# Optimization experiments

Hardware: AMD Instinct MI355X
Metric: run time of the kernel (lower is better)

The kernel has to match this reference:

```python
import jax, jax.numpy as jnp
import numpy as np

N_HEADS = 16

def setup_inputs() -> dict:
    key = jax.random.key(0)
    k1, k2, k3, k4 = jax.random.split(key, 4)
    B, T, C = 2, 2048, 1024
    x = jax.random.normal(k1, (B, T, C), dtype=jnp.float32)
    # torch nn.Linear weights: (out_features, in_features), applied as x @ W.T
    s = 1.0 / np.sqrt(C)
    Wq = jax.random.normal(k2, (C, C), dtype=jnp.float32) * s
    Wk = jax.random.normal(k3, (C, C), dtype=jnp.float32) * s
    Wv = jax.random.normal(k4, (C, C), dtype=jnp.float32) * s
    return {"x": x, "Wq": Wq, "Wk": Wk, "Wv": Wv}

def reference(x, Wq, Wk, Wv):
    B, T, C = x.shape
    H = N_HEADS
    d = C // H
    q = (x @ Wq.T).reshape(B, T, H, d)
    k = (x @ Wk.T).reshape(B, T, H, d)
    v = (x @ Wv.T).reshape(B, T, H, d)
    # NOTE: original scales by full C**-0.5, not per-head dim
    wei = jnp.einsum('bqhd,bkhd->bhqk', q, k) * (C ** -0.5)
    causal = jnp.tril(jnp.ones((T, T), dtype=bool))
    wei = jnp.where(causal, wei, -jnp.inf)
    wei = jax.nn.softmax(wei, axis=-1)
    out = jnp.einsum('bhqk,bkhd->bqhd', wei, v)
    return out.reshape(B, T, C)
```

## Files before the change

kernel.cpp:

```cpp
#include <hip/hip_runtime.h>
#include <math.h>

typedef __attribute__((ext_vector_type(8))) short short8;
typedef __attribute__((ext_vector_type(4))) float f32x4;
typedef __attribute__((ext_vector_type(16))) float f32x16;

#define BDIM 2
#define T_LEN 2048
#define CDIM 1024
#define NH 16
#define DHEAD 64
#define M_ROWS (BDIM * T_LEN)
#define NX (M_ROWS * CDIM)
#define NW (CDIM * CDIM)

#define QSCL 0.045084220f

__device__ inline unsigned short f2bf(float f) {
    union { float f; unsigned u; } v; v.f = f;
    unsigned r = v.u + 0x7fff + ((v.u >> 16) & 1);
    return (unsigned short)(r >> 16);
}

__device__ __forceinline__ void gload16(const unsigned short* g, unsigned short* l) {
    __builtin_amdgcn_global_load_lds(
        (const __attribute__((address_space(1))) void*)g,
        (__attribute__((address_space(3))) void*)l, 16, 0, 0);
}

__global__ __launch_bounds__(256) void conv_bf16(
    const float* __restrict__ x, const float* __restrict__ wq,
    const float* __restrict__ wk, const float* __restrict__ wv,
    unsigned short* __restrict__ dst)
{
    int id = blockIdx.x * 256 + threadIdx.x;
    const float* s;
    float scl = 1.0f;
    if (id < NX / 8) s = x + (size_t)id * 8;
    else {
        int r = id - NX / 8;
        int wsel = r >> 17;
        int off = r & 131071;
        const float* w = (wsel == 0) ? wq : (wsel == 1) ? wk : wv;
        if (wsel == 0) scl = QSCL;
        s = w + (size_t)off * 8;
    }
    float4 a = ((const float4*)s)[0];
    float4 b = ((const float4*)s)[1];
    union { unsigned short u[8]; short8 v; } o;
    o.u[0] = f2bf(a.x * scl); o.u[1] = f2bf(a.y * scl); o.u[2] = f2bf(a.z * scl); o.u[3] = f2bf(a.w * scl);
    o.u[4] = f2bf(b.x * scl); o.u[5] = f2bf(b.y * scl); o.u[6] = f2bf(b.z * scl); o.u[7] = f2bf(b.w * scl);
    *(short8*)(dst + (size_t)id * 8) = o.v;
}

__global__ __launch_bounds__(256) void qkv_gemm_f(
    const unsigned short* __restrict__ xb, const unsigned short* __restrict__ wb,
    unsigned short* __restrict__ qkv)
{
    __shared__ unsigned short sh[17408];
    unsigned short* A = sh;
    unsigned short* Bt = sh + 8192;
    const int z = blockIdx.z;
    const int m0 = blockIdx.x * 128;
    const int n0 = blockIdx.y * 128;
    const int tid = threadIdx.x;
    const int l = tid & 63, w = tid >> 6;
    const int li = l & 15, g4 = l >> 4;
    const int wr = w >> 1, wc = w & 1;

    const unsigned short* wsrc = wb + (size_t)z * NW;
    f32x4 acc[4][4] = {};

    for (int k0 = 0; k0 < CDIM; k0 += 64) {
        __syncthreads();
        #pragma unroll
        for (int s = 0; s < 4; ++s) {
            int c = w * 256 + s * 64 + l;
            int row = c >> 3, wcol = c & 7;
            int sw = wcol ^ (row & 7);
            gload16(xb + (size_t)(m0 + row) * CDIM + k0 + sw * 8, A + (w * 256 + s * 64) * 8);
            gload16(wsrc + (size_t)(n0 + row) * CDIM + k0 + sw * 8, Bt + (w * 256 + s * 64) * 8);
        }
        asm volatile("s_waitcnt vmcnt(0)" ::: "memory");
        __syncthreads();
        __builtin_amdgcn_s_setprio(1);
        #pragma unroll
        for (int ks = 0; ks < 2; ++ks) {
            short8 af[4], bf[4];
            #pragma unroll
            for (int fm = 0; fm < 4; ++fm) {
                int row = wr * 64 + fm * 16 + li;
                int lin = row * 128 + ks * 64 + g4 * 16;
                af[fm] = *(const short8*)((const char*)A + (lin ^ ((row & 7) << 4)));
            }
            #pragma unroll
            for (int fn = 0; fn < 4; ++fn) {
                int row = wc * 64 + fn * 16 + li;
                int lin = row * 128 + ks * 64 + g4 * 16;
                bf[fn] = *(const short8*)((const char*)Bt + (lin ^ ((row & 7) << 4)));
            }
            #pragma unroll
            for (int fm = 0; fm < 4; ++fm)
                #pragma unroll
                for (int fn = 0; fn < 4; ++fn)
                    acc[fm][fn] = __builtin_amdgcn_mfma_f32_16x16x32_bf16(af[fm], bf[fn], acc[fm][fn], 0, 0, 0);
        }
        __builtin_amdgcn_s_setprio(0);
    }
    __syncthreads();

    if (z != 2) {
        unsigned short* outp = qkv + (size_t)z * NX;
        #pragma unroll
        for (int fm = 0; fm < 4; ++fm)
            #pragma unroll
            for (int fn = 0; fn < 4; ++fn)
                #pragma unroll
                for (int r = 0; r < 4; ++r) {
                    int m = m0 + wr * 64 + fm * 16 + g4 * 4 + r;
                    int n = n0 + wc * 64 + fn * 16 + li;
                    int b = m >> 11, t = m & 2047;
                    int h = n >> 6, dd = n & 63;
                    outp[((size_t)(b * NH + h) << 17) + ((size_t)t << 6) + dd] = f2bf(acc[fm][fn][r]);
                }
    } else {
        unsigned short (*T)[136] = (unsigned short(*)[136])sh;
        #pragma unroll
        for (int fm = 0; fm < 4; ++fm)
            #pragma unroll
            for (int fn = 0; fn < 4; ++fn)
                #pragma unroll
                for (int r = 0; r < 4; ++r) {
                    int ml = wr * 64 + fm * 16 + g4 * 4 + r;
                    int nl = wc * 64 + fn * 16 + li;
                    T[nl][ml] = f2bf(acc[fm][fn][r]);
                }
        __syncthreads();
        int b = m0 >> 11;
        int t0 = m0 & 2047;
        unsigned short* vt = qkv + 2 * (size_t)NX;
        #pragma unroll
        for (int s = 0; s < 8; ++s) {
            int row = tid >> 1;
            int col = ((tid & 1) * 8 + s) * 8;
            int ng = n0 + row;
            int h = ng >> 6, dd = ng & 63;
            *(short8*)(vt + ((size_t)(b * NH + h) * 64 + dd) * T_LEN + t0 + col)
                = *(const short8*)&T[row][col];
        }
    }
}

__global__ __launch_bounds__(512, 2) void attn(
    const unsigned short* __restrict__ qkv, float* __restrict__ out)
{
    __shared__ __align__(16) unsigned short KV[2][2][2][8192];

    const int id = blockIdx.x;
    const int half = id >> 8;
    const int rr = id & 255;
    const int tI = rr >> 5;
    const int bx = half ? tI : (15 - tI);
    const int rb = rr & 31;
    const int bh = (rb & 7) * 4 + (rb >> 3);
    const int b = bh >> 4, h = bh & 15;
    const int q0 = bx * 128;
    const int tid = threadIdx.x;
    const int l = tid & 63, w = tid >> 6;
    const int hf = w >> 2, chunk = w & 3;
    const int q31 = l & 31, hi = l >> 5;

    const unsigned short* qp = qkv + (size_t)bh * (T_LEN * DHEAD);
    const unsigned short* kp = qkv + (size_t)NX + (size_t)bh * (T_LEN * DHEAD);
    const unsigned short* vp = qkv + 2 * (size_t)NX + (size_t)bh * (T_LEN * DHEAD);

    const int q0w = q0 + chunk * 32;
    const int qg = q0w + q31;

    short8 aq[4];
    #pragma unroll
    for (int ks = 0; ks < 4; ++ks)
        aq[ks] = *(const short8*)(qp + (size_t)qg * DHEAD + ks * 16 + hi * 8);

    float m_run = -INFINITY, l_run = 0.f;
    f32x16 acc_o[2] = {};

    const int T128 = bx + 1;
    const int hA = (T128 + 1) >> 1;
    const int base = hf ? hA : 0;
    const int lim  = hf ? T128 : hA;
    const int nIt  = hA;
    const int myNt64 = 2 * bx + (chunk >> 1) + 1;

    auto STAGE = [&](int j, int bf) {
        const int kv0 = j * 128;
        #pragma unroll
        for (int s = 0; s < 4; ++s) {
            int g = (chunk * 4 + s) * 64 + l;
            int krow = g >> 3, kc = g & 7;
            int ksw = kc ^ (krow & 7);
            gload16(kp + (size_t)(kv0 + krow) * DHEAD + ksw * 8, &KV[hf][bf][0][(chunk * 4 + s) * 512]);
            int sub = g >> 9, cs = g & 511;
            int vrow = cs >> 3, vc = cs & 7;
            int vsw = vc ^ (vrow & 7);
            gload16(vp + (size_t)vrow * T_LEN + kv0 + sub * 64 + vsw * 8, &KV[hf][bf][1][(chunk * 4 + s) * 512]);
        }
    };

    if (base < lim) STAGE(base, 0);
    asm volatile("s_waitcnt vmcnt(0)" ::: "memory");
    __syncthreads();

    for (int i = 0; i < nIt; ++i) {
        const int cur = i & 1;
        const int myJ = base + i;
        if (myJ + 1 < lim) STAGE(myJ + 1, cur ^ 1);

        #pragma unroll
        for (int sub = 0; sub < 2; ++sub) {
            const int t64 = myJ * 2 + sub;
            if (myJ < lim && t64 < myNt64) {
                const char* Kbase = (const char*)&KV[hf][cur][0][0] + sub * 8192;
                const char* Vbase = (const char*)&KV[hf][cur][1][0] + sub * 8192;
                const int kv0 = t64 * 64;

                f32x16 sacc[2] = {};
                __builtin_amdgcn_s_setprio(1);
                #pragma unroll
                for (int ks = 0; ks < 4; ++ks) {
                    #pragma unroll
                    for (int nb = 0; nb < 2; ++nb) {
                        int row = 32 * nb + q31;
                        int lin = row * 128 + ks * 32 + hi * 16;
                        short8 ak = *(const short8*)(Kbase + (lin ^ ((l & 7) << 4)));
                        sacc[nb] = __builtin_amdgcn_mfma_f32_32x32x16_bf16(ak, aq[ks], sacc[nb], 0, 0, 0);
                    }
                }
                __builtin_amdgcn_s_setprio(0);

                const bool domask = (kv0 + 63 > q0w);
                if (domask) {
                    #pragma unroll
                    for (int nb = 0; nb < 2; ++nb)
                        #pragma unroll
                        for (int r = 0; r < 16; ++r) {
                            int kvg = kv0 + 32 * nb + (r & 3) + 8 * (r >> 2) + 4 * hi;
                            if (kvg > qg) sacc[nb][r] = -INFINITY;
                        }
                }
                float m16[16];
                #pragma unroll
                for (int r = 0; r < 16; ++r) m16[r] = fmaxf(sacc[0][r], sacc[1][r]);
                #pragma unroll
                for (int st = 8; st >= 1; st >>= 1)
                    #pragma unroll
                    for (int r2 = 0; r2 < 8; ++r2)
                        if (r2 < st) m16[r2] = fmaxf(m16[r2], m16[r2 + st]);
                float mloc = fmaxf(m16[0], __shfl_xor(m16[0], 32));

                bool upd = mloc > m_run + 8.0f;
                if (__any(upd)) {
                    float mn = fmaxf(m_run, mloc);
                    float c = exp2f(m_run - mn);
                    l_run *= c;
                    #pragma unroll
                    for (int nb2 = 0; nb2 < 2; ++nb2)
                        #pragma unroll
                        for (int r = 0; r < 16; ++r)
                            acc_o[nb2][r] *= c;
                    m_run = mn;
                }
                float ps[16];
                #pragma unroll
                for (int r = 0; r < 16; ++r) {
                    float p0 = exp2f(sacc[0][r] - m_run);
                    float p1 = exp2f(sacc[1][r] - m_run);
                    sacc[0][r] = p0; sacc[1][r] = p1;
                    ps[r] = p0 + p1;
                }
                #pragma unroll
                for (int st = 8; st >= 1; st >>= 1)
                    #pragma unroll
                    for (int r2 = 0; r2 < 8; ++r2)
                        if (r2 < st) ps[r2] += ps[r2 + st];
                l_run += ps[0] + __shfl_xor(ps[0], 32);

                unsigned dw[16];
                #pragma unroll
                for (int u = 0; u < 16; ++u) {
                    float lo = sacc[u >> 3][(2 * u) & 15];
                    float hif = sacc[u >> 3][((2 * u) & 15) + 1];
                    asm("v_cvt_pk_bf16_f32 %0, %1, %2" : "=v"(dw[u]) : "v"(lo), "v"(hif));
                }

                __builtin_amdgcn_s_setprio(1);
                #pragma unroll
                for (int ks = 0; ks < 4; ++ks) {
                    unsigned a0 = dw[4 * ks],     b0 = dw[4 * ks + 2];
                    unsigned a1 = dw[4 * ks + 1], b1 = dw[4 * ks + 3];
                    asm("v_permlane32_swap_b32 %0, %1" : "+v"(a0), "+v"(b0));
                    asm("v_permlane32_swap_b32 %0, %1" : "+v"(a1), "+v"(b1));
                    union { unsigned u[4]; short8 v; } pb;
                    pb.u[0] = a0; pb.u[1] = a1; pb.u[2] = b0; pb.u[3] = b1;
                    #pragma unroll
                    for (int nb2 = 0; nb2 < 2; ++nb2) {
                        int row = 32 * nb2 + q31;
                        int lin = row * 128 + ks * 32 + hi * 16;
                        short8 av = *(const short8*)(Vbase + (lin ^ ((l & 7) << 4)));
                        acc_o[nb2] = __builtin_amdgcn_mfma_f32_32x32x16_bf16(av, pb.v, acc_o[nb2], 0, 0, 0);
                    }
                }
                __builtin_amdgcn_s_setprio(0);
            }
        }
        asm volatile("s_waitcnt vmcnt(0)" ::: "memory");
        __syncthreads();
    }

    float* MB = (float*)&KV[0][0][0][0];
    float* slot = MB + (chunk * 64 + l) * 34;
    if (hf) {
        #pragma unroll
        for (int nb2 = 0; nb2 < 2; ++nb2)
            #pragma unroll
            for (int r = 0; r < 16; ++r) slot[nb2 * 16 + r] = acc_o[nb2][r];
        slot[32] = m_run; slot[33] = l_run;
    }
    __syncthreads();
    if (!hf) {
        float mB = slot[32], lB = slot[33];
        float m = fmaxf(m_run, mB);
        float cA = exp2f(m_run - m);
        float cB = (mB == -INFINITY) ? 0.f : exp2f(mB - m);
        float inv = 1.0f / (l_run * cA + lB * cB);
        float* ob = out + ((size_t)(b * T_LEN + qg)) * CDIM + h * DHEAD;
        #pragma unroll
        for (int nb2 = 0; nb2 < 2; ++nb2)
            #pragma unroll
            for (int r = 0; r < 16; ++r) {
                int dd = 32 * nb2 + (r & 3) + 8 * (r >> 2) + 4 * hi;
                ob[dd] = (acc_o[nb2][r] * cA + slot[nb2 * 16 + r] * cB) * inv;
            }
    }
}

extern "C" void kernel_launch(void* const* d_in, const int* in_sizes, int n_in,
                              void* d_out, int out_size, void* d_ws, size_t ws_size,
                              hipStream_t stream) {
    const float* x  = (const float*)d_in[0];
    const float* Wq = (const float*)d_in[1];
    const float* Wk = (const float*)d_in[2];
    const float* Wv = (const float*)d_in[3];
    float* out = (float*)d_out;

    unsigned short* xb = (unsigned short*)d_out;
    unsigned short* wb = xb + NX;
    unsigned short* qkv = (unsigned short*)d_ws;

    conv_bf16<<<dim3((NX / 8 + 3 * NW / 8) / 256), dim3(256), 0, stream>>>(x, Wq, Wk, Wv, xb);
    qkv_gemm_f<<<dim3(M_ROWS / 128, CDIM / 128, 3), dim3(256), 0, stream>>>(xb, wb, qkv);
    attn<<<dim3(512), dim3(512), 0, stream>>>(qkv, out);
}
```

Measured before the change: 102.1 us.

## Process full 128-wide KV tile per softmax step with split PV accumulators

Each iteration now computes QK^T scores for the whole 128-key staged tile at once, instead of two sequential 64-key halves. That halves the per-tile max/sum reductions, cross-lane shuffles and rescale checks. The P·V products for the two halves go into separate accumulators, summed at the end, so the two halves' MFMA chains do not depend on each other. In exchange, register pressure rises (four score accumulators plus two output accumulators), and on the diagonal some fully masked 64-key halves are now computed instead of skipped.

```diff
diff --git a/kernel.cpp b/kernel.cpp
--- a/kernel.cpp
+++ b/kernel.cpp
@@ -183,7 +183,8 @@
         aq[ks] = *(const short8*)(qp + (size_t)qg * DHEAD + ks * 16 + hi * 8);
 
     float m_run = -INFINITY, l_run = 0.f;
-    f32x16 acc_o[2] = {};
+    f32x16 acc_oA[2] = {};
+    f32x16 acc_oB[2] = {};
 
     const int T128 = bx + 1;
     const int hA = (T128 + 1) >> 1;
@@ -216,83 +217,87 @@
         const int myJ = base + i;
         if (myJ + 1 < lim) STAGE(myJ + 1, cur ^ 1);
 
-        #pragma unroll
-        for (int sub = 0; sub < 2; ++sub) {
-            const int t64 = myJ * 2 + sub;
-            if (myJ < lim && t64 < myNt64) {
-                const char* Kbase = (const char*)&KV[hf][cur][0][0] + sub * 8192;
-                const char* Vbase = (const char*)&KV[hf][cur][1][0] + sub * 8192;
-                const int kv0 = t64 * 64;
-
-                f32x16 sacc[2] = {};
-                __builtin_amdgcn_s_setprio(1);
-                #pragma unroll
-                for (int ks = 0; ks < 4; ++ks) {
+        if (myJ < lim && 2 * myJ < myNt64) {
+            const char* Kbase = (const char*)&KV[hf][cur][0][0];
+            const char* Vbase = (const char*)&KV[hf][cur][1][0];
+            const int kv0 = myJ * 128;
+
+            f32x16 sacc[4] = {};
+            __builtin_amdgcn_s_setprio(1);
+            #pragma unroll
+            for (int ks = 0; ks < 4; ++ks) {
+                #pragma unroll
+                for (int nb = 0; nb < 4; ++nb) {
+                    int row = 32 * (nb & 1) + q31;
+                    int lin = row * 128 + ks * 32 + hi * 16;
+                    short8 ak = *(const short8*)(Kbase + (nb >> 1) * 8192 + (lin ^ ((l & 7) << 4)));
+                    sacc[nb] = __builtin_amdgcn_mfma_f32_32x32x16_bf16(ak, aq[ks], sacc[nb], 0, 0, 0);
+                }
+            }
+            __builtin_amdgcn_s_setprio(0);
+
+            const bool domask = (kv0 + 127 > q0w);
+            if (domask) {
+                #pragma unroll
+                for (int nb = 0; nb < 4; ++nb)
                     #pragma unroll
-                    for (int nb = 0; nb < 2; ++nb) {
-                        int row = 32 * nb + q31;
-                        int lin = row * 128 + ks * 32 + hi * 16;
-                        short8 ak = *(const short8*)(Kbase + (lin ^ ((l & 7) << 4)));
-                        sacc[nb] = __builtin_amdgcn_mfma_f32_32x32x16_bf16(ak, aq[ks], sacc[nb], 0, 0, 0);
+                    for (int r = 0; r < 16; ++r) {
+                        int kvg = kv0 + 32 * nb + (r & 3) + 8 * (r >> 2) + 4 * hi;
+                        if (kvg > qg) sacc[nb][r] = -INFINITY;
                     }
-                }
-                __builtin_amdgcn_s_setprio(0);
-
-                const bool domask = (kv0 + 63 > q0w);
-                if (domask) {
+            }
+            float m16[16];
+            #pragma unroll
+            for (int r = 0; r < 16; ++r)
+                m16[r] = fmaxf(fmaxf(sacc[0][r], sacc[1][r]), fmaxf(sacc[2][r], sacc[3][r]));
+            #pragma unroll
+            for (int st = 8; st >= 1; st >>= 1)
+                #pragma unroll
+                for (int r2 = 0; r2 < 8; ++r2)
+                    if (r2 < st) m16[r2] = fmaxf(m16[r2], m16[r2 + st]);
+            float mloc = fmaxf(m16[0], __shfl_xor(m16[0], 32));
+
+            bool upd = mloc > m_run + 8.0f;
+            if (__any(upd)) {
+                float mn = fmaxf(m_run, mloc);
+                float c = exp2f(m_run - mn);
+                l_run *= c;
+                #pragma unroll
+                for (int nb2 = 0; nb2 < 2; ++nb2)
                     #pragma unroll
-                    for (int nb = 0; nb < 2; ++nb)
-                        #pragma unroll
-                        for (int r = 0; r < 16; ++r) {
-                            int kvg = kv0 + 32 * nb + (r & 3) + 8 * (r >> 2) + 4 * hi;
-                            if (kvg > qg) sacc[nb][r] = -INFINITY;
-                        }
-                }
-                float m16[16];
-                #pragma unroll
-                for (int r = 0; r < 16; ++r) m16[r] = fmaxf(sacc[0][r], sacc[1][r]);
-                #pragma unroll
-                for (int st = 8; st >= 1; st >>= 1)
-                    #pragma unroll
-                    for (int r2 = 0; r2 < 8; ++r2)
-                        if (r2 < st) m16[r2] = fmaxf(m16[r2], m16[r2 + st]);
-                float mloc = fmaxf(m16[0], __shfl_xor(m16[0], 32));
-
-                bool upd = mloc > m_run + 8.0f;
-                if (__any(upd)) {
-                    float mn = fmaxf(m_run, mloc);
-                    float c = exp2f(m_run - mn);
-                    l_run *= c;
-                    #pragma unroll
-                    for (int nb2 = 0; nb2 < 2; ++nb2)
-                        #pragma unroll
-                        for (int r = 0; r < 16; ++r)
-                            acc_o[nb2][r] *= c;
-                    m_run = mn;
-                }
-                float ps[16];
-                #pragma unroll
-                for (int r = 0; r < 16; ++r) {
-                    float p0 = exp2f(sacc[0][r] - m_run);
-                    float p1 = exp2f(sacc[1][r] - m_run);
-                    sacc[0][r] = p0; sacc[1][r] = p1;
-                    ps[r] = p0 + p1;
-                }
-                #pragma unroll
-                for (int st = 8; st >= 1; st >>= 1)
-                    #pragma unroll
-                    for (int r2 = 0; r2 < 8; ++r2)
-                        if (r2 < st) ps[r2] += ps[r2 + st];
-                l_run += ps[0] + __shfl_xor(ps[0], 32);
-
+                    for (int r = 0; r < 16; ++r) {
+                        acc_oA[nb2][r] *= c;
+                        acc_oB[nb2][r] *= c;
+                    }
+                m_run = mn;
+            }
+            float ps[16];
+            #pragma unroll
+            for (int r = 0; r < 16; ++r) {
+                float p0 = exp2f(sacc[0][r] - m_run);
+                float p1 = exp2f(sacc[1][r] - m_run);
+                float p2 = exp2f(sacc[2][r] - m_run);
+                float p3 = exp2f(sacc[3][r] - m_run);
+                sacc[0][r] = p0; sacc[1][r] = p1; sacc[2][r] = p2; sacc[3][r] = p3;
+                ps[r] = (p0 + p1) + (p2 + p3);
+            }
+            #pragma unroll
+            for (int st = 8; st >= 1; st >>= 1)
+                #pragma unroll
+                for (int r2 = 0; r2 < 8; ++r2)
+                    if (r2 < st) ps[r2] += ps[r2 + st];
+            l_run += ps[0] + __shfl_xor(ps[0], 32);
+
+            #pragma unroll
+            for (int sub = 0; sub < 2; ++sub) {
                 unsigned dw[16];
                 #pragma unroll
                 for (int u = 0; u < 16; ++u) {
-                    float lo = sacc[u >> 3][(2 * u) & 15];
-                    float hif = sacc[u >> 3][((2 * u) & 15) + 1];
+                    float lo = sacc[2 * sub + (u >> 3)][(2 * u) & 15];
+                    float hif = sacc[2 * sub + (u >> 3)][((2 * u) & 15) + 1];
                     asm("v_cvt_pk_bf16_f32 %0, %1, %2" : "=v"(dw[u]) : "v"(lo), "v"(hif));
                 }
-
+                f32x16* accp = sub ? acc_oB : acc_oA;
                 __builtin_amdgcn_s_setprio(1);
                 #pragma unroll
                 for (int ks = 0; ks < 4; ++ks) {
@@ -306,8 +311,8 @@
                     for (int nb2 = 0; nb2 < 2; ++nb2) {
                         int row = 32 * nb2 + q31;
                         int lin = row * 128 + ks * 32 + hi * 16;
-                        short8 av = *(const short8*)(Vbase + (lin ^ ((l & 7) << 4)));
-                        acc_o[nb2] = __builtin_amdgcn_mfma_f32_32x32x16_bf16(av, pb.v, acc_o[nb2], 0, 0, 0);
+                        short8 av = *(const short8*)(Vbase + sub * 8192 + (lin ^ ((l & 7) << 4)));
+                        accp[nb2] = __builtin_amdgcn_mfma_f32_32x32x16_bf16(av, pb.v, accp[nb2], 0, 0, 0);
                     }
                 }
                 __builtin_amdgcn_s_setprio(0);
@@ -316,6 +321,13 @@
         asm volatile("s_waitcnt vmcnt(0)" ::: "memory");
         __syncthreads();
     }
+
+    f32x16 acc_o[2];
+    #pragma unroll
+    for (int nb2 = 0; nb2 < 2; ++nb2)
+        #pragma unroll
+        for (int r = 0; r < 16; ++r)
+            acc_o[nb2][r] = acc_oA[nb2][r] + acc_oB[nb2][r];
 
     float* MB = (float*)&KV[0][0][0][0];
     float* slot = MB + (chunk * 64 + l) * 34;
```

Result: faster. 99.17 us (-2.9%).
